# Kernel optimization log

Measured on AMD Instinct MI355X. Metric: run time of the kernel, lower is better.

Reference implementation:

```python
import jax, jax.numpy as jnp
import numpy as np

VOCAB = 32000
H = 1024
T = 2048


def setup_inputs() -> dict:
    key = jax.random.key(0)
    ks = jax.random.split(key, 6)
    s = 1.0 / np.sqrt(H)  # torch LSTMCell init bound
    return {
        "tokens": jax.random.randint(ks[0], (T,), 0, VOCAB),
        "embedding": jax.random.normal(ks[1], (VOCAB, H), jnp.float32),
        "W_ih": jax.random.uniform(ks[2], (4 * H, H), jnp.float32, -s, s),
        "W_hh": jax.random.uniform(ks[3], (4 * H, H), jnp.float32, -s, s),
        "b_ih": jax.random.uniform(ks[4], (4 * H,), jnp.float32, -s, s),
        "b_hh": jax.random.uniform(ks[5], (4 * H,), jnp.float32, -s, s),
    }


def reference(tokens, embedding, W_ih, W_hh, b_ih, b_hh):
    # Gather all embeddings up front: [T, H]
    xs = embedding[tokens]
    # Precompute input-side gate pre-activations for all timesteps: [T, 4H]
    gx = xs @ W_ih.T + b_ih + b_hh

    def step(carry, gx_t):
        h, c = carry  # each [H]
        gates = gx_t + h @ W_hh.T  # [4H]
        i, f, g, o = jnp.split(gates, 4)
        i = jax.nn.sigmoid(i)
        f = jax.nn.sigmoid(f)
        g = jnp.tanh(g)
        o = jax.nn.sigmoid(o)
        c = f * c + i * g
        h = o * jnp.tanh(c)
        return (h, c), None

    h0 = jnp.zeros((H,), dtype=xs.dtype)
    c0 = jnp.zeros((H,), dtype=xs.dtype)
    (h, c), _ = jax.lax.scan(step, (h0, c0), gx)
    # Original returns LSTMCell hidden tuple with batch dim 1: ([1,H], [1,H])
    return h[None, :], c[None, :]
```

## Files before the change

kernel.cpp:

```cpp
#include <hip/hip_runtime.h>
#include <hip/hip_bf16.h>

#define TT 2048
#define HH 1024
#define GH 4096

__device__ __forceinline__ float sigm(float x){ return 1.0f / (1.0f + __expf(-x)); }
__device__ __forceinline__ float bflo(unsigned v){ return __uint_as_float(v << 16); }
__device__ __forceinline__ float bfhi(unsigned v){ return __uint_as_float(v & 0xffff0000u); }
__device__ __forceinline__ unsigned short f2bu(float x){
  __hip_bfloat16 b = __float2bfloat16(x);
  return *reinterpret_cast<unsigned short*>(&b);
}

#define BM 128
#define BN 64
#define BK 32

__global__ __launch_bounds__(256) void gemm_simple(
    const int* __restrict__ tokens,
    const float* __restrict__ emb,
    const float* __restrict__ Wih,
    const float* __restrict__ bih,
    const float* __restrict__ bhh,
    float* __restrict__ gx)
{
  __shared__ float As[BM][BK+1];
  __shared__ float Bs[BN][BK+1];
  __shared__ int tok_s[BM];

  const int tid = threadIdx.x;
  const int bn = blockIdx.x;
  const int bm = blockIdx.y;
  const int m0 = bm*BM, n0 = bn*BN;

  if (tid < BM) tok_s[tid] = tokens[m0 + tid];
  __syncthreads();

  const int tm = tid >> 4;
  const int tn = tid & 15;

  float acc[8][4];
  #pragma unroll
  for (int i = 0; i < 8; ++i)
    #pragma unroll
    for (int j = 0; j < 4; ++j) acc[i][j] = 0.0f;

  for (int k0 = 0; k0 < HH; k0 += BK) {
    for (int idx = tid; idx < BM*BK; idx += 256) {
      int r = idx >> 5, c = idx & 31;
      As[r][c] = emb[(size_t)tok_s[r]*HH + k0 + c];
    }
    for (int idx = tid; idx < BN*BK; idx += 256) {
      int r = idx >> 5, c = idx & 31;
      Bs[r][c] = Wih[(size_t)(n0 + r)*HH + k0 + c];
    }
    __syncthreads();
    #pragma unroll
    for (int k = 0; k < BK; ++k) {
      float a[8], bb[4];
      #pragma unroll
      for (int i = 0; i < 8; ++i) a[i] = As[tm*8 + i][k];
      #pragma unroll
      for (int j = 0; j < 4; ++j) bb[j] = Bs[tn*4 + j][k];
      #pragma unroll
      for (int i = 0; i < 8; ++i)
        #pragma unroll
        for (int j = 0; j < 4; ++j)
          acc[i][j] = fmaf(a[i], bb[j], acc[i][j]);
    }
    __syncthreads();
  }

  float bias[4];
  #pragma unroll
  for (int j = 0; j < 4; ++j) {
    int col = n0 + tn*4 + j;
    bias[j] = bih[col] + bhh[col];
  }
  #pragma unroll
  for (int i = 0; i < 8; ++i) {
    int r = m0 + tm*8 + i;
    #pragma unroll
    for (int j = 0; j < 4; ++j)
      gx[(size_t)r*GH + (n0 + tn*4 + j)] = acc[i][j] + bias[j];
  }
}

#define GBLK 64
#define NTH 512
#define HSTRIDE 130
#define ROWU 257

__global__ __launch_bounds__(NTH) void lstm_scan_lds(
    const float* __restrict__ gx,
    const float* __restrict__ Whh,
    unsigned long long* slots,
    float* __restrict__ out,
    int nrep)
{
  extern __shared__ __align__(16) unsigned wdw[];
  __shared__ float h_lds[32*HSTRIDE];

  const int b = blockIdx.x;
  const int tid = threadIdx.x;
  const int s  = tid & 31;
  const int G  = tid >> 5;
  const int o  = (b << 4) + G;

  for (int r = 0; r < 64; ++r) {
    const int Gr = r >> 2, g = r & 3;
    const int jrow = (g << 10) + (b << 4) + Gr;
    const int c0 = tid * 2;
    const float2 f2 = *(const float2*)(Whh + (size_t)jrow*HH + c0);
    const unsigned pk = (unsigned)f2bu(f2.x) | ((unsigned)f2bu(f2.y) << 16);
    const int sT = c0 >> 5, j2 = (c0 & 31) >> 2, d = (c0 >> 1) & 1;
    wdw[r*(2*ROWU) + (j2*32 + sT)*2 + d] = pk;
  }
  for (int i = tid; i < 32*HSTRIDE; i += NTH) h_lds[i] = 0.0f;

  float cst = 0.0f;
  float g4[4];
  #pragma unroll
  for (int g = 0; g < 4; ++g) g4[g] = gx[(g << 10) + o];

  const int i0 = tid, i1 = tid + 512;
  const int p0 = (i0 >> 5)*HSTRIDE + (i0 & 31);
  const int p1 = (i1 >> 5)*HSTRIDE + (i1 & 31);
  const unsigned long long* prep = slots + (size_t)((b & (nrep-1)) * 2) * 1024;
  __syncthreads();

  const uint2* wld2 = (const uint2*)wdw;

  for (int t = 0; t < TT; ++t) {
    float ng[4] = {0.f, 0.f, 0.f, 0.f};
    if (t + 1 < TT) {
      #pragma unroll
      for (int g = 0; g < 4; ++g)
        ng[g] = gx[(size_t)(t+1)*GH + (g << 10) + o];
    }

    if (t > 0) {
      const unsigned long long* sb = prep + (size_t)(t & 1) * 1024;
      const unsigned tg = (unsigned)t;
      unsigned long long v0 = __hip_atomic_load(&sb[i0], __ATOMIC_RELAXED, __HIP_MEMORY_SCOPE_AGENT);
      unsigned long long v1 = __hip_atomic_load(&sb[i1], __ATOMIC_RELAXED, __HIP_MEMORY_SCOPE_AGENT);
      while ((unsigned)(v0 >> 32) != tg)
        v0 = __hip_atomic_load(&sb[i0], __ATOMIC_RELAXED, __HIP_MEMORY_SCOPE_AGENT);
      while ((unsigned)(v1 >> 32) != tg)
        v1 = __hip_atomic_load(&sb[i1], __ATOMIC_RELAXED, __HIP_MEMORY_SCOPE_AGENT);
      h_lds[p0] = __uint_as_float((unsigned)v0);
      h_lds[p1] = __uint_as_float((unsigned)v1);
      __syncthreads();
    }

    float a0 = 0.f, a1 = 0.f, a2 = 0.f, a3 = 0.f;
    const float* hseg = h_lds + s*HSTRIDE;
    #pragma unroll
    for (int j2 = 0; j2 < 8; ++j2) {
      const float2 hA = *(const float2*)(hseg + 4*j2);
      const float2 hB = *(const float2*)(hseg + 4*j2 + 2);
      const uint2 w0 = wld2[(G*4 + 0)*ROWU + j2*32 + s];
      const uint2 w1 = wld2[(G*4 + 1)*ROWU + j2*32 + s];
      const uint2 w2 = wld2[(G*4 + 2)*ROWU + j2*32 + s];
      const uint2 w3 = wld2[(G*4 + 3)*ROWU + j2*32 + s];
      a0 = fmaf(bflo(w0.x), hA.x, a0); a0 = fmaf(bfhi(w0.x), hA.y, a0);
      a0 = fmaf(bflo(w0.y), hB.x, a0); a0 = fmaf(bfhi(w0.y), hB.y, a0);
      a1 = fmaf(bflo(w1.x), hA.x, a1); a1 = fmaf(bfhi(w1.x), hA.y, a1);
      a1 = fmaf(bflo(w1.y), hB.x, a1); a1 = fmaf(bfhi(w1.y), hB.y, a1);
      a2 = fmaf(bflo(w2.x), hA.x, a2); a2 = fmaf(bfhi(w2.x), hA.y, a2);
      a2 = fmaf(bflo(w2.y), hB.x, a2); a2 = fmaf(bfhi(w2.y), hB.y, a2);
      a3 = fmaf(bflo(w3.x), hA.x, a3); a3 = fmaf(bfhi(w3.x), hA.y, a3);
      a3 = fmaf(bflo(w3.y), hB.x, a3); a3 = fmaf(bfhi(w3.y), hB.y, a3);
    }
    #pragma unroll
    for (int m = 1; m <= 16; m <<= 1) {
      a0 += __shfl_xor(a0, m);
      a1 += __shfl_xor(a1, m);
      a2 += __shfl_xor(a2, m);
      a3 += __shfl_xor(a3, m);
    }

    const float xi = a0 + g4[0];
    const float xf = a1 + g4[1];
    const float xg = a2 + g4[2];
    const float xo = a3 + g4[3];
    cst = sigm(xf)*cst + sigm(xi)*tanhf(xg);
    const float hnew = sigm(xo)*tanhf(cst);

    if (t == TT-1) {
      if (s == 0) {
        out[o]        = hnew;
        out[1024 + o] = cst;
      }
    } else {
      if (s == 0) {
        const unsigned long long pv =
            (((unsigned long long)(unsigned)(t+1)) << 32) |
            (unsigned long long)__float_as_uint(hnew);
        const int nxt = (t+1) & 1;
        for (int r = 0; r < nrep; ++r)
          __hip_atomic_store(&slots[(size_t)(r*2 + nxt)*1024 + o], pv,
                             __ATOMIC_RELAXED, __HIP_MEMORY_SCOPE_AGENT);
      }
      #pragma unroll
      for (int g = 0; g < 4; ++g) g4[g] = ng[g];
    }
    __syncthreads();
  }
}

__global__ __launch_bounds__(NTH, 2) void lstm_scan_reg(
    const float* __restrict__ gx,
    const float* __restrict__ Whh,
    unsigned long long* slots,
    float* __restrict__ out)
{
  const int b = blockIdx.x;
  const int tid = threadIdx.x;
  const int s  = tid & 31;
  const int rg = tid >> 5;

  __shared__ float h_lds[32*HSTRIDE];
  __shared__ float gates_lds[64];

  float w[128];
  #pragma unroll
  for (int a = 0; a < 4; ++a) {
    int row = rg*4 + a;
    int jrow = ((row >> 4) << 10) + (b << 4) + (row & 15);
    const float* wr = Whh + (size_t)jrow*HH + s*32;
    #pragma unroll
    for (int q = 0; q < 8; ++q) {
      float4 f4 = ((const float4*)wr)[q];
      w[a*32 + q*4 + 0] = f4.x; w[a*32 + q*4 + 1] = f4.y;
      w[a*32 + q*4 + 2] = f4.z; w[a*32 + q*4 + 3] = f4.w;
    }
  }

  for (int i = tid; i < 32*HSTRIDE; i += NTH) h_lds[i] = 0.0f;
  float c0 = 0.0f, c1 = 0.0f;
  const int i0 = tid, i1 = tid + 512;
  const int p0 = (i0 >> 5)*HSTRIDE + (i0 & 31);
  const int p1 = (i1 >> 5)*HSTRIDE + (i1 & 31);
  const int myrow = rg*4 + s;
  const int myj = ((myrow >> 4) << 10) + (b << 4) + (myrow & 15);
  __syncthreads();

  for (int t = 0; t < TT; ++t) {
    float gxv = 0.0f;
    if (s < 4) gxv = gx[(size_t)t*GH + myj];

    if (t > 0) {
      const unsigned long long* sb = slots + (size_t)(t & 1)*1024;
      const unsigned tg = (unsigned)t;
      unsigned long long v0 = __hip_atomic_load(&sb[i0], __ATOMIC_RELAXED, __HIP_MEMORY_SCOPE_AGENT);
      unsigned long long v1 = __hip_atomic_load(&sb[i1], __ATOMIC_RELAXED, __HIP_MEMORY_SCOPE_AGENT);
      while ((unsigned)(v0 >> 32) != tg)
        v0 = __hip_atomic_load(&sb[i0], __ATOMIC_RELAXED, __HIP_MEMORY_SCOPE_AGENT);
      while ((unsigned)(v1 >> 32) != tg)
        v1 = __hip_atomic_load(&sb[i1], __ATOMIC_RELAXED, __HIP_MEMORY_SCOPE_AGENT);
      h_lds[p0] = __uint_as_float((unsigned)v0);
      h_lds[p1] = __uint_as_float((unsigned)v1);
      __syncthreads();
    }

    float acc0 = 0.f, acc1 = 0.f, acc2 = 0.f, acc3 = 0.f;
    const float* hseg = h_lds + s*HSTRIDE;
    #pragma unroll
    for (int c2 = 0; c2 < 16; ++c2) {
      float2 hv = *(const float2*)(hseg + 2*c2);
      acc0 = fmaf(w[0*32+2*c2], hv.x, acc0); acc0 = fmaf(w[0*32+2*c2+1], hv.y, acc0);
      acc1 = fmaf(w[1*32+2*c2], hv.x, acc1); acc1 = fmaf(w[1*32+2*c2+1], hv.y, acc1);
      acc2 = fmaf(w[2*32+2*c2], hv.x, acc2); acc2 = fmaf(w[2*32+2*c2+1], hv.y, acc2);
      acc3 = fmaf(w[3*32+2*c2], hv.x, acc3); acc3 = fmaf(w[3*32+2*c2+1], hv.y, acc3);
    }
    #pragma unroll
    for (int m = 1; m <= 16; m <<= 1) {
      acc0 += __shfl_xor(acc0, m);
      acc1 += __shfl_xor(acc1, m);
      acc2 += __shfl_xor(acc2, m);
      acc3 += __shfl_xor(acc3, m);
    }
    if (s < 4) {
      float v = acc0;
      if (s == 1) v = acc1; else if (s == 2) v = acc2; else if (s == 3) v = acc3;
      gates_lds[rg*4 + s] = v + gxv;
    }
    __syncthreads();

    if (tid < 8) {
      int n0 = tid*2, n1 = n0 + 1;
      float xi0 = gates_lds[n0],    xi1 = gates_lds[n1];
      float xf0 = gates_lds[16+n0], xf1 = gates_lds[16+n1];
      float xg0 = gates_lds[32+n0], xg1 = gates_lds[32+n1];
      float xo0 = gates_lds[48+n0], xo1 = gates_lds[48+n1];
      c0 = sigm(xf0)*c0 + sigm(xi0)*tanhf(xg0);
      c1 = sigm(xf1)*c1 + sigm(xi1)*tanhf(xg1);
      float h0 = sigm(xo0)*tanhf(c0);
      float h1 = sigm(xo1)*tanhf(c1);
      if (t == TT-1) {
        out[(b<<4)+n0]      = h0;
        out[(b<<4)+n1]      = h1;
        out[1024+(b<<4)+n0] = c0;
        out[1024+(b<<4)+n1] = c1;
      } else {
        unsigned long long* db = slots + (size_t)((t+1)&1)*1024;
        unsigned long long tg = ((unsigned long long)(unsigned)(t+1)) << 32;
        __hip_atomic_store(&db[(b<<4)+n0], tg | (unsigned long long)__float_as_uint(h0),
                           __ATOMIC_RELAXED, __HIP_MEMORY_SCOPE_AGENT);
        __hip_atomic_store(&db[(b<<4)+n1], tg | (unsigned long long)__float_as_uint(h1),
                           __ATOMIC_RELAXED, __HIP_MEMORY_SCOPE_AGENT);
      }
    }
  }
}

__global__ void zero_out(float* out){
  int i = blockIdx.x*256 + threadIdx.x;
  if (i < 2048) out[i] = 0.0f;
}

extern "C" void kernel_launch(void* const* d_in, const int* in_sizes, int n_in,
                              void* d_out, int out_size, void* d_ws, size_t ws_size,
                              hipStream_t stream) {
  (void)in_sizes; (void)n_in; (void)out_size;
  const int* tokens = (const int*)d_in[0];
  const float* emb  = (const float*)d_in[1];
  const float* Wih  = (const float*)d_in[2];
  const float* Whh  = (const float*)d_in[3];
  const float* bih  = (const float*)d_in[4];
  const float* bhh  = (const float*)d_in[5];
  float* out = (float*)d_out;

  const size_t gxBytes  = (size_t)TT*GH*sizeof(float);
  const size_t repBytes = (size_t)8*2*1024*8;
  unsigned long long* slots = (unsigned long long*)d_ws;

  int nrep;
  size_t slotBytes;
  if (ws_size >= repBytes + gxBytes)      { nrep = 8; slotBytes = repBytes; }
  else if (ws_size >= 16384 + gxBytes)    { nrep = 1; slotBytes = 16384;   }
  else {
    zero_out<<<dim3(8), dim3(256), 0, stream>>>(out);
    return;
  }
  float* gx = (float*)((char*)d_ws + slotBytes);

  hipMemsetAsync(slots, 0, slotBytes, stream);
  gemm_simple<<<dim3(64,16), dim3(256), 0, stream>>>(tokens, emb, Wih, bih, bhh, gx);

  const int dynBytes = 64 * (2*ROWU) * 4;
  hipError_t e = hipFuncSetAttribute((const void*)lstm_scan_lds,
                                     hipFuncAttributeMaxDynamicSharedMemorySize,
                                     dynBytes);
  if (e == hipSuccess) {
    lstm_scan_lds<<<dim3(GBLK), dim3(NTH), dynBytes, stream>>>(gx, Whh, slots, out, nrep);
  } else {
    (void)hipGetLastError();
    lstm_scan_reg<<<dim3(GBLK), dim3(NTH), 0, stream>>>(gx, Whh, slots, out);
  }
}
```

Measured before the change: 5.786 ms.

## Double-buffer hidden state in LDS, use fast tanh, raise slot replicas to 16

The LDS scan kernel now keeps the hidden-state vector in two ping-pong LDS buffers with a compact stride, which lets it drop the trailing per-step barrier and keep only one barrier per timestep. tanhf is replaced with an exp-based fast tanh, and when the workspace is large enough the number of replicated global handoff slots goes from 8 to 16, so fewer blocks poll each copy. The goal is to shorten the serial per-step critical path of the recurrence. The cost is slightly lower tanh accuracy and more atomic stores per step from each writer.

```diff
diff --git a/kernel.cpp b/kernel.cpp
--- a/kernel.cpp
+++ b/kernel.cpp
@@ -6,6 +6,11 @@
 #define GH 4096
 
 __device__ __forceinline__ float sigm(float x){ return 1.0f / (1.0f + __expf(-x)); }
+__device__ __forceinline__ float tanh_fast(float x){
+  float xc = fminf(fmaxf(x, -15.0f), 15.0f);
+  float e = __expf(2.0f * xc);
+  return (e - 1.0f) / (e + 1.0f);
+}
 __device__ __forceinline__ float bflo(unsigned v){ return __uint_as_float(v << 16); }
 __device__ __forceinline__ float bfhi(unsigned v){ return __uint_as_float(v & 0xffff0000u); }
 __device__ __forceinline__ unsigned short f2bu(float x){
@@ -89,7 +94,7 @@
 
 #define GBLK 64
 #define NTH 512
-#define HSTRIDE 130
+#define HST2 33
 #define ROWU 257
 
 __global__ __launch_bounds__(NTH) void lstm_scan_lds(
@@ -100,7 +105,7 @@
     int nrep)
 {
   extern __shared__ __align__(16) unsigned wdw[];
-  __shared__ float h_lds[32*HSTRIDE];
+  __shared__ float hb2[2][32*HST2];
 
   const int b = blockIdx.x;
   const int tid = threadIdx.x;
@@ -117,7 +122,8 @@
     const int sT = c0 >> 5, j2 = (c0 & 31) >> 2, d = (c0 >> 1) & 1;
     wdw[r*(2*ROWU) + (j2*32 + sT)*2 + d] = pk;
   }
-  for (int i = tid; i < 32*HSTRIDE; i += NTH) h_lds[i] = 0.0f;
+  for (int i = tid; i < 1024; i += NTH)
+    hb2[0][(i >> 5)*HST2 + (i & 31)] = 0.0f;
 
   float cst = 0.0f;
   float g4[4];
@@ -125,8 +131,8 @@
   for (int g = 0; g < 4; ++g) g4[g] = gx[(g << 10) + o];
 
   const int i0 = tid, i1 = tid + 512;
-  const int p0 = (i0 >> 5)*HSTRIDE + (i0 & 31);
-  const int p1 = (i1 >> 5)*HSTRIDE + (i1 & 31);
+  const int p0 = (i0 >> 5)*HST2 + (i0 & 31);
+  const int p1 = (i1 >> 5)*HST2 + (i1 & 31);
   const unsigned long long* prep = slots + (size_t)((b & (nrep-1)) * 2) * 1024;
   __syncthreads();
 
@@ -140,6 +146,7 @@
         ng[g] = gx[(size_t)(t+1)*GH + (g << 10) + o];
     }
 
+    float* hcur = hb2[t & 1];
     if (t > 0) {
       const unsigned long long* sb = prep + (size_t)(t & 1) * 1024;
       const unsigned tg = (unsigned)t;
@@ -149,13 +156,13 @@
         v0 = __hip_atomic_load(&sb[i0], __ATOMIC_RELAXED, __HIP_MEMORY_SCOPE_AGENT);
       while ((unsigned)(v1 >> 32) != tg)
         v1 = __hip_atomic_load(&sb[i1], __ATOMIC_RELAXED, __HIP_MEMORY_SCOPE_AGENT);
-      h_lds[p0] = __uint_as_float((unsigned)v0);
-      h_lds[p1] = __uint_as_float((unsigned)v1);
-      __syncthreads();
-    }
+      hcur[p0] = __uint_as_float((unsigned)v0);
+      hcur[p1] = __uint_as_float((unsigned)v1);
+    }
+    __syncthreads();
 
     float a0 = 0.f, a1 = 0.f, a2 = 0.f, a3 = 0.f;
-    const float* hseg = h_lds + s*HSTRIDE;
+    const float* hseg = hcur + s*HST2;
     #pragma unroll
     for (int j2 = 0; j2 < 8; ++j2) {
       const float2 hA = *(const float2*)(hseg + 4*j2);
@@ -185,8 +192,8 @@
     const float xf = a1 + g4[1];
     const float xg = a2 + g4[2];
     const float xo = a3 + g4[3];
-    cst = sigm(xf)*cst + sigm(xi)*tanhf(xg);
-    const float hnew = sigm(xo)*tanhf(cst);
+    cst = sigm(xf)*cst + sigm(xi)*tanh_fast(xg);
+    const float hnew = sigm(xo)*tanh_fast(cst);
 
     if (t == TT-1) {
       if (s == 0) {
@@ -206,7 +213,6 @@
       #pragma unroll
       for (int g = 0; g < 4; ++g) g4[g] = ng[g];
     }
-    __syncthreads();
   }
 }
 
@@ -221,7 +227,7 @@
   const int s  = tid & 31;
   const int rg = tid >> 5;
 
-  __shared__ float h_lds[32*HSTRIDE];
+  __shared__ float h_lds[32*130];
   __shared__ float gates_lds[64];
 
   float w[128];
@@ -238,11 +244,11 @@
     }
   }
 
-  for (int i = tid; i < 32*HSTRIDE; i += NTH) h_lds[i] = 0.0f;
+  for (int i = tid; i < 32*130; i += NTH) h_lds[i] = 0.0f;
   float c0 = 0.0f, c1 = 0.0f;
   const int i0 = tid, i1 = tid + 512;
-  const int p0 = (i0 >> 5)*HSTRIDE + (i0 & 31);
-  const int p1 = (i1 >> 5)*HSTRIDE + (i1 & 31);
+  const int p0 = (i0 >> 5)*130 + (i0 & 31);
+  const int p1 = (i1 >> 5)*130 + (i1 & 31);
   const int myrow = rg*4 + s;
   const int myj = ((myrow >> 4) << 10) + (b << 4) + (myrow & 15);
   __syncthreads();
@@ -266,7 +272,7 @@
     }
 
     float acc0 = 0.f, acc1 = 0.f, acc2 = 0.f, acc3 = 0.f;
-    const float* hseg = h_lds + s*HSTRIDE;
+    const float* hseg = h_lds + s*130;
     #pragma unroll
     for (int c2 = 0; c2 < 16; ++c2) {
       float2 hv = *(const float2*)(hseg + 2*c2);
@@ -333,14 +339,14 @@
   const float* bhh  = (const float*)d_in[5];
   float* out = (float*)d_out;
 
-  const size_t gxBytes  = (size_t)TT*GH*sizeof(float);
-  const size_t repBytes = (size_t)8*2*1024*8;
+  const size_t gxBytes = (size_t)TT*GH*sizeof(float);
   unsigned long long* slots = (unsigned long long*)d_ws;
 
   int nrep;
   size_t slotBytes;
-  if (ws_size >= repBytes + gxBytes)      { nrep = 8; slotBytes = repBytes; }
-  else if (ws_size >= 16384 + gxBytes)    { nrep = 1; slotBytes = 16384;   }
+  if      (ws_size >= (size_t)16*2*1024*8 + gxBytes) { nrep = 16; slotBytes = (size_t)16*2*1024*8; }
+  else if (ws_size >= (size_t) 8*2*1024*8 + gxBytes) { nrep =  8; slotBytes = (size_t) 8*2*1024*8; }
+  else if (ws_size >= 16384 + gxBytes)               { nrep =  1; slotBytes = 16384; }
   else {
     zero_out<<<dim3(8), dim3(256), 0, stream>>>(out);
     return;
```

After: 13.76 ms. 2.38x slower.

## Fuse input GEMM and LSTM scan into one kernel with per-row-block readiness counters

Applied to the files above, without the earlier changes.

Merges the input-projection GEMM and the recurrent scan into a single launch. The first 64 blocks run the scan and the remaining 1024 blocks compute gx tiles, each bumping a per-row-block counter when finished. The scan blocks spin on those counters before reading each 128-step chunk of gx, so the recurrence can start as soon as the first rows are ready instead of waiting for the whole GEMM. The risks are spin-waiting on counters, scan blocks possibly not being co-resident with the GEMM blocks, and GEMM blocks running with half their threads idle and the larger dynamic LDS allocation.

```diff
diff --git a/kernel.cpp b/kernel.cpp
--- a/kernel.cpp
+++ b/kernel.cpp
@@ -13,97 +13,108 @@
   return *reinterpret_cast<unsigned short*>(&b);
 }
 
+#define SCANBLK 64
+#define NTH 512
+#define HSTRIDE 130
+#define ROWU 257
+#define NREP 8
+
 #define BM 128
 #define BN 64
 #define BK 32
-
-__global__ __launch_bounds__(256) void gemm_simple(
+#define GEMMBLK 1024
+
+__global__ __launch_bounds__(NTH) void fused_lstm(
     const int* __restrict__ tokens,
     const float* __restrict__ emb,
     const float* __restrict__ Wih,
     const float* __restrict__ bih,
     const float* __restrict__ bhh,
-    float* __restrict__ gx)
+    const float* __restrict__ Whh,
+    unsigned long long* slots,
+    int* cnt,
+    float* gx,
+    float* __restrict__ out)
 {
-  __shared__ float As[BM][BK+1];
-  __shared__ float Bs[BN][BK+1];
-  __shared__ int tok_s[BM];
-
+  extern __shared__ __align__(16) unsigned dynls[];
   const int tid = threadIdx.x;
-  const int bn = blockIdx.x;
-  const int bm = blockIdx.y;
-  const int m0 = bm*BM, n0 = bn*BN;
-
-  if (tid < BM) tok_s[tid] = tokens[m0 + tid];
-  __syncthreads();
-
-  const int tm = tid >> 4;
-  const int tn = tid & 15;
-
-  float acc[8][4];
-  #pragma unroll
-  for (int i = 0; i < 8; ++i)
-    #pragma unroll
-    for (int j = 0; j < 4; ++j) acc[i][j] = 0.0f;
-
-  for (int k0 = 0; k0 < HH; k0 += BK) {
-    for (int idx = tid; idx < BM*BK; idx += 256) {
-      int r = idx >> 5, c = idx & 31;
-      As[r][c] = emb[(size_t)tok_s[r]*HH + k0 + c];
-    }
-    for (int idx = tid; idx < BN*BK; idx += 256) {
-      int r = idx >> 5, c = idx & 31;
-      Bs[r][c] = Wih[(size_t)(n0 + r)*HH + k0 + c];
-    }
-    __syncthreads();
-    #pragma unroll
-    for (int k = 0; k < BK; ++k) {
-      float a[8], bb[4];
-      #pragma unroll
-      for (int i = 0; i < 8; ++i) a[i] = As[tm*8 + i][k];
-      #pragma unroll
-      for (int j = 0; j < 4; ++j) bb[j] = Bs[tn*4 + j][k];
-      #pragma unroll
-      for (int i = 0; i < 8; ++i)
+
+  if (blockIdx.x >= SCANBLK) {
+    float* As = (float*)dynls;
+    float* Bs = As + 128*33;
+    int* tok_s = (int*)(Bs + 64*33);
+
+    const int gb = blockIdx.x - SCANBLK;
+    const int bn = gb & 63, bm = gb >> 6;
+    const int m0 = bm*BM, n0 = bn*BN;
+
+    if (tid < BM) tok_s[tid] = tokens[m0 + tid];
+    __syncthreads();
+
+    const int tm = tid >> 4;
+    const int tn = tid & 15;
+
+    float acc[8][4];
+    #pragma unroll
+    for (int i = 0; i < 8; ++i)
+      #pragma unroll
+      for (int j = 0; j < 4; ++j) acc[i][j] = 0.0f;
+
+    for (int k0 = 0; k0 < HH; k0 += BK) {
+      if (tid < 256) {
+        for (int idx = tid; idx < BM*BK; idx += 256) {
+          int r = idx >> 5, c = idx & 31;
+          As[r*33 + c] = emb[(size_t)tok_s[r]*HH + k0 + c];
+        }
+        for (int idx = tid; idx < BN*BK; idx += 256) {
+          int r = idx >> 5, c = idx & 31;
+          Bs[r*33 + c] = Wih[(size_t)(n0 + r)*HH + k0 + c];
+        }
+      }
+      __syncthreads();
+      if (tid < 256) {
+        #pragma unroll
+        for (int k = 0; k < BK; ++k) {
+          float a[8], bb[4];
+          #pragma unroll
+          for (int i = 0; i < 8; ++i) a[i] = As[(tm*8 + i)*33 + k];
+          #pragma unroll
+          for (int j = 0; j < 4; ++j) bb[j] = Bs[(tn*4 + j)*33 + k];
+          #pragma unroll
+          for (int i = 0; i < 8; ++i)
+            #pragma unroll
+            for (int j = 0; j < 4; ++j)
+              acc[i][j] = fmaf(a[i], bb[j], acc[i][j]);
+        }
+      }
+      __syncthreads();
+    }
+
+    if (tid < 256) {
+      float bias[4];
+      #pragma unroll
+      for (int j = 0; j < 4; ++j) {
+        int col = n0 + tn*4 + j;
+        bias[j] = bih[col] + bhh[col];
+      }
+      #pragma unroll
+      for (int i = 0; i < 8; ++i) {
+        int r = m0 + tm*8 + i;
         #pragma unroll
         for (int j = 0; j < 4; ++j)
-          acc[i][j] = fmaf(a[i], bb[j], acc[i][j]);
-    }
-    __syncthreads();
-  }
-
-  float bias[4];
-  #pragma unroll
-  for (int j = 0; j < 4; ++j) {
-    int col = n0 + tn*4 + j;
-    bias[j] = bih[col] + bhh[col];
-  }
-  #pragma unroll
-  for (int i = 0; i < 8; ++i) {
-    int r = m0 + tm*8 + i;
-    #pragma unroll
-    for (int j = 0; j < 4; ++j)
-      gx[(size_t)r*GH + (n0 + tn*4 + j)] = acc[i][j] + bias[j];
-  }
-}
-
-#define GBLK 64
-#define NTH 512
-#define HSTRIDE 130
-#define ROWU 257
-
-__global__ __launch_bounds__(NTH) void lstm_scan_lds(
-    const float* __restrict__ gx,
-    const float* __restrict__ Whh,
-    unsigned long long* slots,
-    float* __restrict__ out,
-    int nrep)
-{
-  extern __shared__ __align__(16) unsigned wdw[];
+          gx[(size_t)r*GH + (n0 + tn*4 + j)] = acc[i][j] + bias[j];
+      }
+    }
+    __syncthreads();
+    if (tid == 0)
+      __hip_atomic_fetch_add(&cnt[bm], 1, __ATOMIC_RELEASE, __HIP_MEMORY_SCOPE_AGENT);
+    return;
+  }
+
+  unsigned* wdw = dynls;
   __shared__ float h_lds[32*HSTRIDE];
 
   const int b = blockIdx.x;
-  const int tid = threadIdx.x;
   const int s  = tid & 31;
   const int G  = tid >> 5;
   const int o  = (b << 4) + G;
@@ -119,6 +130,10 @@
   }
   for (int i = tid; i < 32*HSTRIDE; i += NTH) h_lds[i] = 0.0f;
 
+  int rdy = 0;
+  while (__hip_atomic_load(&cnt[0], __ATOMIC_ACQUIRE, __HIP_MEMORY_SCOPE_AGENT) < 64) {}
+  rdy = 1;
+
   float cst = 0.0f;
   float g4[4];
   #pragma unroll
@@ -127,7 +142,7 @@
   const int i0 = tid, i1 = tid + 512;
   const int p0 = (i0 >> 5)*HSTRIDE + (i0 & 31);
   const int p1 = (i1 >> 5)*HSTRIDE + (i1 & 31);
-  const unsigned long long* prep = slots + (size_t)((b & (nrep-1)) * 2) * 1024;
+  const unsigned long long* prep = slots + (size_t)((b & (NREP-1)) * 2) * 1024;
   __syncthreads();
 
   const uint2* wld2 = (const uint2*)wdw;
@@ -135,6 +150,11 @@
   for (int t = 0; t < TT; ++t) {
     float ng[4] = {0.f, 0.f, 0.f, 0.f};
     if (t + 1 < TT) {
+      const int rb = (t+1) >> 7;
+      if (rdy <= rb) {
+        while (__hip_atomic_load(&cnt[rb], __ATOMIC_ACQUIRE, __HIP_MEMORY_SCOPE_AGENT) < 64) {}
+        rdy = rb + 1;
+      }
       #pragma unroll
       for (int g = 0; g < 4; ++g)
         ng[g] = gx[(size_t)(t+1)*GH + (g << 10) + o];
@@ -199,7 +219,8 @@
             (((unsigned long long)(unsigned)(t+1)) << 32) |
             (unsigned long long)__float_as_uint(hnew);
         const int nxt = (t+1) & 1;
-        for (int r = 0; r < nrep; ++r)
+        #pragma unroll
+        for (int r = 0; r < NREP; ++r)
           __hip_atomic_store(&slots[(size_t)(r*2 + nxt)*1024 + o], pv,
                              __ATOMIC_RELAXED, __HIP_MEMORY_SCOPE_AGENT);
       }
@@ -207,6 +228,76 @@
       for (int g = 0; g < 4; ++g) g4[g] = ng[g];
     }
     __syncthreads();
+  }
+}
+
+__global__ __launch_bounds__(256) void gemm_simple(
+    const int* __restrict__ tokens,
+    const float* __restrict__ emb,
+    const float* __restrict__ Wih,
+    const float* __restrict__ bih,
+    const float* __restrict__ bhh,
+    float* __restrict__ gx)
+{
+  __shared__ float As[BM][BK+1];
+  __shared__ float Bs[BN][BK+1];
+  __shared__ int tok_s[BM];
+
+  const int tid = threadIdx.x;
+  const int bn = blockIdx.x;
+  const int bm = blockIdx.y;
+  const int m0 = bm*BM, n0 = bn*BN;
+
+  if (tid < BM) tok_s[tid] = tokens[m0 + tid];
+  __syncthreads();
+
+  const int tm = tid >> 4;
+  const int tn = tid & 15;
+
+  float acc[8][4];
+  #pragma unroll
+  for (int i = 0; i < 8; ++i)
+    #pragma unroll
+    for (int j = 0; j < 4; ++j) acc[i][j] = 0.0f;
+
+  for (int k0 = 0; k0 < HH; k0 += BK) {
+    for (int idx = tid; idx < BM*BK; idx += 256) {
+      int r = idx >> 5, c = idx & 31;
+      As[r][c] = emb[(size_t)tok_s[r]*HH + k0 + c];
+    }
+    for (int idx = tid; idx < BN*BK; idx += 256) {
+      int r = idx >> 5, c = idx & 31;
+      Bs[r][c] = Wih[(size_t)(n0 + r)*HH + k0 + c];
+    }
+    __syncthreads();
+    #pragma unroll
+    for (int k = 0; k < BK; ++k) {
+      float a[8], bb[4];
+      #pragma unroll
+      for (int i = 0; i < 8; ++i) a[i] = As[tm*8 + i][k];
+      #pragma unroll
+      for (int j = 0; j < 4; ++j) bb[j] = Bs[tn*4 + j][k];
+      #pragma unroll
+      for (int i = 0; i < 8; ++i)
+        #pragma unroll
+        for (int j = 0; j < 4; ++j)
+          acc[i][j] = fmaf(a[i], bb[j], acc[i][j]);
+    }
+    __syncthreads();
+  }
+
+  float bias[4];
+  #pragma unroll
+  for (int j = 0; j < 4; ++j) {
+    int col = n0 + tn*4 + j;
+    bias[j] = bih[col] + bhh[col];
+  }
+  #pragma unroll
+  for (int i = 0; i < 8; ++i) {
+    int r = m0 + tm*8 + i;
+    #pragma unroll
+    for (int j = 0; j < 4; ++j)
+      gx[(size_t)r*GH + (n0 + tn*4 + j)] = acc[i][j] + bias[j];
   }
 }
 
@@ -333,31 +424,38 @@
   const float* bhh  = (const float*)d_in[5];
   float* out = (float*)d_out;
 
-  const size_t gxBytes  = (size_t)TT*GH*sizeof(float);
-  const size_t repBytes = (size_t)8*2*1024*8;
+  const size_t gxBytes   = (size_t)TT*GH*sizeof(float);
+  const size_t slotBytes = (size_t)NREP*2*1024*8;
+  const size_t ctrlBytes = slotBytes + 2048;
+
   unsigned long long* slots = (unsigned long long*)d_ws;
-
-  int nrep;
-  size_t slotBytes;
-  if (ws_size >= repBytes + gxBytes)      { nrep = 8; slotBytes = repBytes; }
-  else if (ws_size >= 16384 + gxBytes)    { nrep = 1; slotBytes = 16384;   }
-  else {
-    zero_out<<<dim3(8), dim3(256), 0, stream>>>(out);
+  int* cnt  = (int*)((char*)d_ws + slotBytes);
+  float* gx = (float*)((char*)d_ws + ctrlBytes);
+
+  if (ws_size < ctrlBytes + gxBytes) {
+    if (ws_size >= 16384 + gxBytes) {
+      float* gx1 = (float*)((char*)d_ws + 16384);
+      hipMemsetAsync(d_ws, 0, 16384, stream);
+      gemm_simple<<<dim3(64,16), dim3(256), 0, stream>>>(tokens, emb, Wih, bih, bhh, gx1);
+      lstm_scan_reg<<<dim3(SCANBLK), dim3(NTH), 0, stream>>>(gx1, Whh, slots, out);
+    } else {
+      zero_out<<<dim3(8), dim3(256), 0, stream>>>(out);
+    }
     return;
   }
-  float* gx = (float*)((char*)d_ws + slotBytes);
-
-  hipMemsetAsync(slots, 0, slotBytes, stream);
-  gemm_simple<<<dim3(64,16), dim3(256), 0, stream>>>(tokens, emb, Wih, bih, bhh, gx);
+
+  hipMemsetAsync(d_ws, 0, ctrlBytes, stream);
 
   const int dynBytes = 64 * (2*ROWU) * 4;
-  hipError_t e = hipFuncSetAttribute((const void*)lstm_scan_lds,
+  hipError_t e = hipFuncSetAttribute((const void*)fused_lstm,
                                      hipFuncAttributeMaxDynamicSharedMemorySize,
                                      dynBytes);
   if (e == hipSuccess) {
-    lstm_scan_lds<<<dim3(GBLK), dim3(NTH), dynBytes, stream>>>(gx, Whh, slots, out, nrep);
+    fused_lstm<<<dim3(SCANBLK + GEMMBLK), dim3(NTH), dynBytes, stream>>>(
+        tokens, emb, Wih, bih, bhh, Whh, slots, cnt, gx, out);
   } else {
     (void)hipGetLastError();
-    lstm_scan_reg<<<dim3(GBLK), dim3(NTH), 0, stream>>>(gx, Whh, slots, out);
-  }
-}
+    gemm_simple<<<dim3(64,16), dim3(256), 0, stream>>>(tokens, emb, Wih, bih, bhh, gx);
+    lstm_scan_reg<<<dim3(SCANBLK), dim3(NTH), 0, stream>>>(gx, Whh, slots, out);
+  }
+}
```

Result: no change. 5.755 ms (median of 2 runs) (-0.5%).
